# Kernel tuning notes

Measured on AMD Instinct MI355X. Metric: run time of the kernel, lower is better.

Reference implementation:

```python
import jax, jax.numpy as jnp
import numpy as np

B, SEQ, D, H = 16, 100, 128, 8
NS = SEQ + 1
HD = D // H
LN_EPS = 1e-5
NEG_INF = -1e9
GAMMA = 1.0


def setup_inputs() -> dict:
    key = jax.random.key(0)
    ks = jax.random.split(key, 16)
    s = 1.0 / np.sqrt(D)
    return {
        "desc_embeddings": jax.random.normal(ks[0], (B, SEQ, D), jnp.float32),
        "name_value_embeddings": jax.random.normal(ks[1], (B, NS, D), jnp.float32),
        "mask_M": jax.random.uniform(ks[2], (B, H, SEQ, SEQ), jnp.float32),
        "Wq": jax.random.normal(ks[3], (D, D), jnp.float32) * s,
        "bq": jnp.zeros((D,), jnp.float32),
        "Wk": jax.random.normal(ks[4], (D, D), jnp.float32) * s,
        "bk": jnp.zeros((D,), jnp.float32),
        "Wv": jax.random.normal(ks[5], (D, D), jnp.float32) * s,
        "bv": jnp.zeros((D,), jnp.float32),
        "W1": jax.random.normal(ks[6], (D, 2 * D), jnp.float32) * s,  # edge_update lin1
        "b1": jnp.zeros((D,), jnp.float32),
        "ln_g": jnp.ones((D,), jnp.float32),
        "ln_b": jnp.zeros((D,), jnp.float32),
        "W2": jax.random.normal(ks[7], (D, D), jnp.float32) * s,  # edge_update lin2
        "b2": jnp.zeros((D,), jnp.float32),
        "Wa": jax.random.normal(ks[8], (1, 3 * HD), jnp.float32) * s,  # attn_proj
        "ba": jnp.zeros((1,), jnp.float32),
    }


def _layernorm(x, g, b):
    mu = x.mean(-1, keepdims=True)
    var = ((x - mu) ** 2).mean(-1, keepdims=True)
    return (x - mu) * jax.lax.rsqrt(var + LN_EPS) * g + b


def reference(desc_embeddings, name_value_embeddings, mask_M,
              Wq, bq, Wk, bk, Wv, bv, W1, b1, ln_g, ln_b, W2, b2, Wa, ba):
    # structural adjacency: CLS->Var on, Var->CLS off, Var-Var without self loops
    var_adj = 1.0 - jnp.eye(SEQ, dtype=jnp.float32)
    adj = jnp.zeros((NS, NS), jnp.float32)
    adj = adj.at[1:, 1:].set(var_adj).at[0, 1:].set(1.0)  # [NS, NS]

    def proj(W, b_):
        return (name_value_embeddings @ W.T + b_).reshape(B, NS, H, HD).transpose(0, 2, 1, 3)

    q, k, v = proj(Wq, bq), proj(Wk, bk), proj(Wv, bv)  # [B, H, NS, HD]

    # edge features: broadcast-concat of desc embeddings, [B, NS, NS, 2D]
    d = desc_embeddings
    var_edge = jnp.concatenate([
        jnp.broadcast_to(d[:, :, None, :], (B, SEQ, SEQ, D)),
        jnp.broadcast_to(d[:, None, :, :], (B, SEQ, SEQ, D))], axis=-1)
    cls_edge = jnp.concatenate([d, d], axis=-1)  # [B, SEQ, 2D]
    edge = jnp.zeros((B, NS, NS, 2 * D), jnp.float32)
    edge = edge.at[:, 1:, 1:].set(var_edge).at[:, 0, 1:].set(cls_edge).at[:, 1:, 0].set(cls_edge)

    # edge_update MLP: Linear -> LayerNorm -> ReLU -> Linear
    h = _layernorm(edge @ W1.T + b1, ln_g, ln_b)
    e = jax.nn.relu(h) @ W2.T + b2  # [B, NS, NS, D]
    e = e.reshape(B, NS, NS, H, HD).transpose(0, 3, 1, 2, 4)  # [B, H, NS, NS, HD]
    e = e * adj[None, None, :, :, None]

    qke = jnp.concatenate([
        jnp.broadcast_to(q[:, :, :, None, :], (B, H, NS, NS, HD)),
        jnp.broadcast_to(k[:, :, None, :, :], (B, H, NS, NS, HD)),
        e], axis=-1)  # [B, H, NS, NS, 3*HD]
    qke = jax.nn.leaky_relu(qke, 0.01)  # gat_v2
    logits = jnp.einsum('bhijd,d->bhij', qke, Wa[0]) + ba[0]

    # mask_M probability -> logit bias on Var-Var block
    p = jnp.clip(mask_M, 1e-6, 1.0 - 1e-6)
    bias = (jnp.log(p) - jnp.log1p(-p)) * GAMMA
    logits = logits.at[:, :, 1:, 1:].add(bias)

    logits = logits + jnp.where(adj == 0, NEG_INF, 0.0)[None, None]
    attn = jax.nn.softmax(logits, axis=-1)  # [B, H, NS, NS]
    ctx = jnp.einsum('bhij,bhjd->bhid', attn, v)
    basis = ctx.transpose(0, 2, 1, 3)  # [B, NS, H, HD]
    return basis, attn
```

## Files before the change

kernel.cpp:

```cpp
#include <hip/hip_runtime.h>
#include <hip/hip_bf16.h>

namespace {

constexpr int kB = 16;
constexpr int kSEQ = 100;
constexpr int kNS = 101;
constexpr int kD = 128;
constexpr int kH = 8;

typedef __attribute__((ext_vector_type(8))) __bf16 bf16x8;
typedef __attribute__((ext_vector_type(4))) float f32x4;

__device__ __forceinline__ unsigned short f2bf(float f) {
  union { float f; unsigned int u; } c;
  c.f = f;
  unsigned int u = c.u;
  u += 0x7FFFu + ((u >> 16) & 1u);
  return (unsigned short)(u >> 16);
}

__device__ __forceinline__ float leaky(float x) {
  return x > 0.f ? x : 0.01f * x;
}

__device__ __forceinline__ bf16x8 pack8(const float* y) {
  bf16x8 r;
  r[0] = (__bf16)y[0]; r[1] = (__bf16)y[1];
  r[2] = (__bf16)y[2]; r[3] = (__bf16)y[3];
  r[4] = (__bf16)y[4]; r[5] = (__bf16)y[5];
  r[6] = (__bf16)y[6]; r[7] = (__bf16)y[7];
  return r;
}

__global__ __launch_bounds__(256) void k_front(
    const float* __restrict__ nve,
    const float* __restrict__ Wq, const float* __restrict__ bq,
    const float* __restrict__ Wk, const float* __restrict__ bk,
    const float* __restrict__ Wv, const float* __restrict__ bv,
    const float* __restrict__ Wa,
    const float* __restrict__ desc, const float* __restrict__ W1,
    const float* __restrict__ b1, const float* __restrict__ W2,
    float* __restrict__ v, float* __restrict__ sq, float* __restrict__ sk,
    float* __restrict__ U, float* __restrict__ Qm,
    float* __restrict__ su_, float* __restrict__ nu_,
    float* __restrict__ sw_, float* __restrict__ nw_,
    unsigned short* __restrict__ W2bf) {
  __shared__ float X[8][128];
  __shared__ float part[4][4][4];
  const int bid = blockIdx.x;
  const int tid = threadIdx.x;

  if (bid < 208) {
    const int b = bid / 13;
    const int n0 = (bid % 13) * 8;
    const int d = tid & 127, rh = tid >> 7;
    {
      int r = tid >> 5, c = (tid & 31) * 4;
      int n = n0 + r; if (n > 100) n = 100;
      *(float4*)&X[r][c] = *(const float4*)&nve[((size_t)(b * kNS + n)) * kD + c];
    }
    __syncthreads();

    float aq[4], ak[4], av[4];
    const float bqv = bq[d], bkv = bk[d], bvv = bv[d];
    #pragma unroll
    for (int r = 0; r < 4; ++r) { aq[r] = bqv; ak[r] = bkv; av[r] = bvv; }

    const float* wqr = Wq + (size_t)d * kD;
    const float* wkr = Wk + (size_t)d * kD;
    const float* wvr = Wv + (size_t)d * kD;
    for (int kk = 0; kk < kD; ++kk) {
      float wq = wqr[kk], wk = wkr[kk], wv = wvr[kk];
      #pragma unroll
      for (int r = 0; r < 4; ++r) {
        float x = X[rh * 4 + r][kk];
        aq[r] += wq * x;
        ak[r] += wk * x;
        av[r] += wv * x;
      }
    }

    const int t = d & 15, h = d >> 4;
    const float waq = Wa[t], wak = Wa[16 + t];
    #pragma unroll
    for (int r = 0; r < 4; ++r) {
      int n = n0 + rh * 4 + r;
      if (n < kNS) {
        v[((size_t)(b * kNS + n)) * kD + d] = av[r];
        float cq = leaky(aq[r]) * waq;
        float ck = leaky(ak[r]) * wak;
        cq += __shfl_xor(cq, 1); ck += __shfl_xor(ck, 1);
        cq += __shfl_xor(cq, 2); ck += __shfl_xor(ck, 2);
        cq += __shfl_xor(cq, 4); ck += __shfl_xor(ck, 4);
        cq += __shfl_xor(cq, 8); ck += __shfl_xor(ck, 8);
        if (t == 0) {
          sq[(b * kH + h) * kNS + n] = cq;
          sk[(b * kH + h) * kNS + n] = ck;
        }
      }
    }
  } else if (bid < 416) {
    const int id = bid - 208;
    const int b = id / 13;
    const int s0 = (id % 13) * 8;
    const int d = tid & 127, rh = tid >> 7;
    const int lane = tid & 63, wv = tid >> 6;
    {
      int r = tid >> 5, c = (tid & 31) * 4;
      int s = s0 + r; if (s > 99) s = 99;
      *(float4*)&X[r][c] = *(const float4*)&desc[((size_t)(b * kSEQ + s)) * kD + c];
    }
    __syncthreads();

    float aU[4], aQ[4];
    const float b1v = b1[d];
    #pragma unroll
    for (int r = 0; r < 4; ++r) { aU[r] = b1v; aQ[r] = 0.f; }

    const float* w1r = W1 + (size_t)d * (2 * kD);
    for (int kk = 0; kk < kD; ++kk) {
      float wa = w1r[kk], wb = w1r[kD + kk];
      #pragma unroll
      for (int r = 0; r < 4; ++r) {
        float x = X[rh * 4 + r][kk];
        aU[r] += wa * x;
        aQ[r] += wb * x;
      }
    }
    #pragma unroll
    for (int r = 0; r < 4; ++r) {
      int s = s0 + rh * 4 + r;
      if (s < kSEQ) {
        size_t base = ((size_t)(b * kSEQ + s)) * kD + d;
        U[base] = aU[r];
        Qm[base] = aQ[r];
      }
    }
    #pragma unroll
    for (int r = 0; r < 4; ++r) {
      float s1 = aU[r], s2 = aU[r] * aU[r], s3 = aQ[r], s4 = aQ[r] * aQ[r];
      #pragma unroll
      for (int m = 1; m < 64; m <<= 1) {
        s1 += __shfl_xor(s1, m);
        s2 += __shfl_xor(s2, m);
        s3 += __shfl_xor(s3, m);
        s4 += __shfl_xor(s4, m);
      }
      if (lane == 0) {
        part[wv][r][0] = s1; part[wv][r][1] = s2;
        part[wv][r][2] = s3; part[wv][r][3] = s4;
      }
    }
    __syncthreads();
    if (tid < 32) {
      int r = tid & 7, st = tid >> 3;
      int rh2 = r >> 2, rl = r & 3;
      float val = part[rh2 * 2][rl][st] + part[rh2 * 2 + 1][rl][st];
      int s = s0 + r;
      if (s < kSEQ) {
        float* dst = (st == 0) ? su_ : (st == 1) ? nu_ : (st == 2) ? sw_ : nw_;
        dst[b * kSEQ + s] = val;
      }
    }
  } else {
    int idx = (bid - 416) * 256 + tid;
    W2bf[idx] = f2bf(W2[idx]);
  }
}

__global__ __launch_bounds__(256) void k_g(
    const float* __restrict__ U, const float* __restrict__ Qm,
    float* __restrict__ G) {
  const int it = blockIdx.x;
  const int b = blockIdx.y;
  const int tid = threadIdx.x;
  const int lane = tid & 63, w = tid >> 6;
  const int lr = lane & 15, lg = lane >> 4;

  __shared__ __align__(16) unsigned short Ubf[16 * 128];
  __shared__ __align__(16) unsigned short Qbf[112 * 128];

  {
    int f = tid * 8;
    int row = f >> 7, col = f & 127;
    int i1 = it * 16 + row; if (i1 > 99) i1 = 99;
    const float* src = &U[((size_t)(b * kSEQ + i1)) * kD + col];
    float y[8];
    *(float4*)&y[0] = *(const float4*)&src[0];
    *(float4*)&y[4] = *(const float4*)&src[4];
    *(bf16x8*)&Ubf[row * 128 + ((((col >> 3) ^ (row & 15))) << 3)] = pack8(y);
  }
  for (int itr = 0; itr < 7; ++itr) {
    int f = (itr * 256 + tid) * 8;
    int row = f >> 7, col = f & 127;
    int j1 = row; if (j1 > 99) j1 = 99;
    const float* src = &Qm[((size_t)(b * kSEQ + j1)) * kD + col];
    float y[8];
    *(float4*)&y[0] = *(const float4*)&src[0];
    *(float4*)&y[4] = *(const float4*)&src[4];
    *(bf16x8*)&Qbf[row * 128 + ((((col >> 3) ^ (row & 15))) << 3)] = pack8(y);
  }
  __syncthreads();

  bf16x8 Af[4];
  #pragma unroll
  for (int ks = 0; ks < 4; ++ks) {
    int g8 = (ks * 4 + lg) ^ (lr & 15);
    Af[ks] = *(const bf16x8*)&Ubf[lr * 128 + g8 * 8];
  }
  for (int pass = 0; pass < 2; ++pass) {
    int nth = w + pass * 4;
    if (nth >= 7) break;
    int brow = nth * 16 + lr;
    f32x4 acc = {0.f, 0.f, 0.f, 0.f};
    #pragma unroll
    for (int ks = 0; ks < 4; ++ks) {
      int g8 = (ks * 4 + lg) ^ (brow & 15);
      bf16x8 Bf = *(const bf16x8*)&Qbf[brow * 128 + g8 * 8];
      acc = __builtin_amdgcn_mfma_f32_16x16x32_bf16(Af[ks], Bf, acc, 0, 0, 0);
    }
    #pragma unroll
    for (int r = 0; r < 4; ++r) {
      int i1 = it * 16 + 4 * lg + r;
      if (i1 <= 99)
        G[((size_t)(b * kSEQ + i1)) * 112 + nth * 16 + lr] = acc[r];
    }
  }
}

__global__ __launch_bounds__(256) void k_mid(
    const float* __restrict__ U, const float* __restrict__ Qm,
    const float* __restrict__ G,
    const float* __restrict__ su_, const float* __restrict__ nu_,
    const float* __restrict__ sw_, const float* __restrict__ nw_,
    const unsigned short* __restrict__ W2bf,
    const float* __restrict__ lng, const float* __restrict__ lnb,
    const float* __restrict__ b2, const float* __restrict__ Wa,
    float* __restrict__ SE) {
  const int bid = blockIdx.x;
  const int tid = threadIdx.x;
  const int lane = tid & 63, w = tid >> 6;
  const int lr = lane & 15, lg = lane >> 4;

  __shared__ __align__(16) unsigned short W2sh[128 * 128];
  __shared__ __align__(16) float gsh[128], bsh[128], b2sh[128];
  __shared__ float SEsh0[16][8];

  #pragma unroll
  for (int itr = 0; itr < 8; ++itr) {
    uint4 val = ((const uint4*)W2bf)[itr * 256 + tid];
    int f = (itr * 256 + tid) * 8;
    int row = f >> 7, g8 = (f >> 3) & 15;
    *(uint4*)&W2sh[row * 128 + ((g8 ^ (row & 15)) << 3)] = val;
  }
  if (tid < 128) {
    gsh[tid] = lng[tid];
    b2sh[tid] = b2[tid];
  } else {
    bsh[tid - 128] = lnb[tid - 128];
  }

  if (bid < 1600) {
    const int i0 = bid % 100;
    const int b = bid / 100;

    const float* Urow = U + ((size_t)(b * kSEQ + i0)) * kD;
    float Ureg[32];
    #pragma unroll
    for (int ks = 0; ks < 4; ++ks) {
      int off = ks * 32 + lg * 8;
      *(float4*)&Ureg[ks * 8] = *(const float4*)&Urow[off];
      *(float4*)&Ureg[ks * 8 + 4] = *(const float4*)&Urow[off + 4];
    }
    const float suv = su_[b * kSEQ + i0], nuv = nu_[b * kSEQ + i0];
    float wa4[4];
    *(float4*)wa4 = *(const float4*)&Wa[32 + 4 * lg];
    __syncthreads();

    #pragma unroll
    for (int t = 0; t < 2; ++t) {
      const int jt = w + t * 4;
      if (jt > 6) break;
      const int j1 = jt * 16 + lr;
      const int j1c = j1 > 99 ? 99 : j1;
      const float swv = sw_[b * kSEQ + j1c];
      const float nwv = nw_[b * kSEQ + j1c];
      const float gv = G[((size_t)(b * kSEQ + i0)) * 112 + j1c];
      const float mean = (suv + swv) * (1.f / 128.f);
      const float ex2 = (nuv + nwv + 2.f * gv) * (1.f / 128.f);
      const float var = ex2 - mean * mean;
      const float rstd = rsqrtf(var + 1e-5f);
      const float amul = rstd, aadd = -mean * rstd;

      bf16x8 Bf[4];
      const float* Qrow = Qm + ((size_t)(b * kSEQ + j1c)) * kD;
      #pragma unroll
      for (int ks = 0; ks < 4; ++ks) {
        const int off = ks * 32 + lg * 8;
        float qv[8], gg[8], bb[8], ys[8];
        *(float4*)&qv[0] = *(const float4*)&Qrow[off];
        *(float4*)&qv[4] = *(const float4*)&Qrow[off + 4];
        *(float4*)&gg[0] = *(const float4*)&gsh[off];
        *(float4*)&gg[4] = *(const float4*)&gsh[off + 4];
        *(float4*)&bb[0] = *(const float4*)&bsh[off];
        *(float4*)&bb[4] = *(const float4*)&bsh[off + 4];
        #pragma unroll
        for (int ee = 0; ee < 8; ++ee) {
          float x = Ureg[ks * 8 + ee] + qv[ee];
          float tt = __builtin_fmaf(x, amul, aadd);
          ys[ee] = fmaxf(__builtin_fmaf(tt, gg[ee], bb[ee]), 0.f);
        }
        Bf[ks] = pack8(ys);
      }

      #pragma unroll
      for (int h = 0; h < 8; ++h) {
        f32x4 acc = *(const f32x4*)&b2sh[h * 16 + 4 * lg];
        #pragma unroll
        for (int ks = 0; ks < 4; ++ks) {
          const int row = h * 16 + lr;
          const int g8 = (ks * 4 + lg) ^ lr;
          bf16x8 Af = *(const bf16x8*)&W2sh[row * 128 + g8 * 8];
          acc = __builtin_amdgcn_mfma_f32_16x16x32_bf16(Af, Bf[ks], acc, 0, 0, 0);
        }
        float s = 0.f;
        #pragma unroll
        for (int r = 0; r < 4; ++r) s += leaky(acc[r]) * wa4[r];
        s += __shfl_xor(s, 16);
        s += __shfl_xor(s, 32);
        if (lane < 16 && j1 <= 99)
          SE[(((size_t)(b * kH + h)) * kNS + (i0 + 1)) * kNS + (j1 + 1)] = s;
      }
    }
  } else {
    const int id = bid - 1600;
    const int jt = id % 7;
    const int b = id / 7;

    const int j1 = jt * 16 + lr;
    const int j1c = j1 > 99 ? 99 : j1;
    const float* Urow = U + ((size_t)(b * kSEQ + j1c)) * kD;
    const float* Qrow = Qm + ((size_t)(b * kSEQ + j1c)) * kD;
    float Xreg[32];
    #pragma unroll
    for (int ks = 0; ks < 4; ++ks) {
      int off = ks * 32 + lg * 8;
      float4 ua = *(const float4*)&Urow[off];
      float4 ub = *(const float4*)&Urow[off + 4];
      float4 qa = *(const float4*)&Qrow[off];
      float4 qb = *(const float4*)&Qrow[off + 4];
      Xreg[ks * 8 + 0] = ua.x + qa.x; Xreg[ks * 8 + 1] = ua.y + qa.y;
      Xreg[ks * 8 + 2] = ua.z + qa.z; Xreg[ks * 8 + 3] = ua.w + qa.w;
      Xreg[ks * 8 + 4] = ub.x + qb.x; Xreg[ks * 8 + 5] = ub.y + qb.y;
      Xreg[ks * 8 + 6] = ub.z + qb.z; Xreg[ks * 8 + 7] = ub.w + qb.w;
    }
    float amul, aadd;
    {
      float mean = (su_[b * kSEQ + j1c] + sw_[b * kSEQ + j1c]) * (1.f / 128.f);
      float gd = G[((size_t)(b * kSEQ + j1c)) * 112 + j1c];
      float ex2 = (nu_[b * kSEQ + j1c] + nw_[b * kSEQ + j1c] + 2.f * gd) * (1.f / 128.f);
      float var = ex2 - mean * mean;
      float rstd = rsqrtf(var + 1e-5f);
      amul = rstd; aadd = -mean * rstd;
    }
    __syncthreads();

    bf16x8 Af[4];
    #pragma unroll
    for (int ks = 0; ks < 4; ++ks) {
      float ys[8], gg[8], bb[8];
      const int off = ks * 32 + lg * 8;
      *(float4*)&gg[0] = *(const float4*)&gsh[off];
      *(float4*)&gg[4] = *(const float4*)&gsh[off + 4];
      *(float4*)&bb[0] = *(const float4*)&bsh[off];
      *(float4*)&bb[4] = *(const float4*)&bsh[off + 4];
      #pragma unroll
      for (int ee = 0; ee < 8; ++ee) {
        float t = __builtin_fmaf(Xreg[ks * 8 + ee], amul, aadd);
        ys[ee] = fmaxf(__builtin_fmaf(t, gg[ee], bb[ee]), 0.f);
      }
      Af[ks] = pack8(ys);
    }

    const float waE = Wa[32 + lr];
    #pragma unroll
    for (int n = 0; n < 2; ++n) {
      const int nt = 2 * w + n;
      const int brow = nt * 16 + lr;
      f32x4 acc = {0.f, 0.f, 0.f, 0.f};
      #pragma unroll
      for (int ks = 0; ks < 4; ++ks) {
        int g8 = (ks * 4 + lg) ^ (brow & 15);
        bf16x8 Bf = *(const bf16x8*)&W2sh[brow * 128 + g8 * 8];
        acc = __builtin_amdgcn_mfma_f32_16x16x32_bf16(Af[ks], Bf, acc, 0, 0, 0);
      }
      const float b2v = b2sh[nt * 16 + lr];
      #pragma unroll
      for (int r = 0; r < 4; ++r) {
        float y = acc[r] + b2v;
        float c = leaky(y) * waE;
        c += __shfl_xor(c, 1);
        c += __shfl_xor(c, 2);
        c += __shfl_xor(c, 4);
        c += __shfl_xor(c, 8);
        if (lr == 0) SEsh0[4 * lg + r][nt] = c;
      }
    }
    __syncthreads();
    if (tid < 128) {
      int rowloc = tid & 15, h = tid >> 4;
      int j1o = jt * 16 + rowloc;
      if (j1o <= 99)
        SE[(((size_t)(b * kH + h)) * kNS) * kNS + (j1o + 1)] = SEsh0[rowloc][h];
    }
  }
}

__global__ __launch_bounds__(512) void k_sm(
    const float* __restrict__ sq, const float* __restrict__ sk,
    const float* __restrict__ v, const float* __restrict__ maskM,
    const float* __restrict__ ba,
    float* __restrict__ basis, float* __restrict__ attn) {
  const int h = blockIdx.x;
  const int b = blockIdx.y;
  const int half = blockIdx.z;
  const int tid = threadIdx.x;
  const int lane = tid & 63, w = tid >> 6;

  __shared__ float vsh[101][17];
  __shared__ float scr[8][104];

  for (int j = tid >> 4; j < kNS; j += 32)
    vsh[j][tid & 15] = v[((size_t)(b * kNS + j)) * kD + h * 16 + (tid & 15)];
  __syncthreads();

  const float bav = ba[0];
  const int skbase = (b * kH + h) * kNS;
  const int iend = half * 51 + 51 < kNS ? half * 51 + 51 : kNS;
  for (int i = half * 51 + w; i < iend; i += 8) {
    const float sqv = sq[skbase + i];
    float* arow = attn + (((size_t)(b * kH + h)) * kNS + i) * kNS;
    const int j1 = lane + 1;
    const int j2 = lane + 65;
    const bool val1 = (j1 != i);
    const bool val2 = (j2 <= 100) && (j2 != i);
    float l1 = -1e30f, l2 = -1e30f;
    {
      float lgt = sqv + sk[skbase + j1] + arow[j1] + bav;
      if (i >= 1) {
        float p = maskM[(((size_t)(b * kH + h)) * kSEQ + (i - 1)) * kSEQ + (j1 - 1)];
        p = fminf(fmaxf(p, 1e-6f), 1.f - 1e-6f);
        lgt += __logf(__fdividef(p, 1.f - p));
      }
      if (val1) l1 = lgt;
    }
    if (val2) {
      float lgt = sqv + sk[skbase + j2] + arow[j2] + bav;
      if (i >= 1) {
        float p = maskM[(((size_t)(b * kH + h)) * kSEQ + (i - 1)) * kSEQ + (j2 - 1)];
        p = fminf(fmaxf(p, 1e-6f), 1.f - 1e-6f);
        lgt += __logf(__fdividef(p, 1.f - p));
      }
      l2 = lgt;
    }
    float mx = fmaxf(l1, l2);
    #pragma unroll
    for (int m = 1; m < 64; m <<= 1) mx = fmaxf(mx, __shfl_xor(mx, m));
    float e1 = __expf(l1 - mx);
    float e2 = __expf(l2 - mx);
    float sm = e1 + e2;
    #pragma unroll
    for (int m = 1; m < 64; m <<= 1) sm += __shfl_xor(sm, m);
    float inv = 1.f / sm;
    float a1 = e1 * inv, a2 = e2 * inv;
    arow[j1] = a1;
    scr[w][j1] = a1;
    if (lane < 36) {
      arow[j2] = a2;
      scr[w][j2] = a2;
    }
    if (lane == 0) arow[0] = 0.f;

    const int g = lane >> 4, t = lane & 15;
    float accc = 0.f;
    #pragma unroll 5
    for (int jj = 0; jj < 25; ++jj) {
      int j = 1 + g + jj * 4;
      accc += scr[w][j] * vsh[j][t];
    }
    accc += __shfl_xor(accc, 16);
    accc += __shfl_xor(accc, 32);
    if (lane < 16) basis[(((size_t)(b * kNS + i)) * kH + h) * 16 + t] = accc;
  }
}

}

extern "C" void kernel_launch(void* const* d_in, const int* in_sizes, int n_in,
                              void* d_out, int out_size, void* d_ws,
                              size_t ws_size, hipStream_t stream) {
  const float* desc = (const float*)d_in[0];
  const float* nve = (const float*)d_in[1];
  const float* maskM = (const float*)d_in[2];
  const float* Wq = (const float*)d_in[3];
  const float* bq = (const float*)d_in[4];
  const float* Wk = (const float*)d_in[5];
  const float* bk = (const float*)d_in[6];
  const float* Wv = (const float*)d_in[7];
  const float* bv = (const float*)d_in[8];
  const float* W1 = (const float*)d_in[9];
  const float* b1 = (const float*)d_in[10];
  const float* lng = (const float*)d_in[11];
  const float* lnb = (const float*)d_in[12];
  const float* W2 = (const float*)d_in[13];
  const float* b2 = (const float*)d_in[14];
  const float* Wa = (const float*)d_in[15];
  const float* ba = (const float*)d_in[16];

  float* wsf = (float*)d_ws;
  float* U = wsf;
  float* Qm = U + kB * kSEQ * kD;
  float* vw = Qm + kB * kSEQ * kD;
  float* sqw = vw + kB * kNS * kD;
  float* skw = sqw + kB * kH * kNS;
  float* su_ = skw + kB * kH * kNS;
  float* nu_ = su_ + kB * kSEQ;
  float* sw_ = nu_ + kB * kSEQ;
  float* nw_ = sw_ + kB * kSEQ;
  float* G = nw_ + kB * kSEQ;
  unsigned short* W2bf = (unsigned short*)(G + kB * kSEQ * 112);

  float* basis = (float*)d_out;
  float* attn = basis + (size_t)kB * kNS * kH * 16;
  float* SE = attn;

  k_front<<<dim3(480), 256, 0, stream>>>(nve, Wq, bq, Wk, bk, Wv, bv, Wa,
                                         desc, W1, b1, W2,
                                         vw, sqw, skw, U, Qm,
                                         su_, nu_, sw_, nw_, W2bf);
  k_g<<<dim3(7, kB), 256, 0, stream>>>(U, Qm, G);
  k_mid<<<dim3(1712), 256, 0, stream>>>(U, Qm, G, su_, nu_, sw_, nw_, W2bf,
                                        lng, lnb, b2, Wa, SE);
  k_sm<<<dim3(kH, kB, 2), 512, 0, stream>>>(sqw, skw, vw, maskM, ba,
                                            basis, attn);
}
```

Measured before the change: 74.98 us.

## Fuse edge-MLP logits kernel with softmax/context kernel per query row

New measurement: 92.99 us. +24.0%, slower.

```diff
diff --git a/kernel.cpp b/kernel.cpp
--- a/kernel.cpp
+++ b/kernel.cpp
@@ -229,7 +229,7 @@
   }
 }
 
-__global__ __launch_bounds__(256) void k_mid(
+__global__ __launch_bounds__(256) void k_att(
     const float* __restrict__ U, const float* __restrict__ Qm,
     const float* __restrict__ G,
     const float* __restrict__ su_, const float* __restrict__ nu_,
@@ -237,15 +237,21 @@
     const unsigned short* __restrict__ W2bf,
     const float* __restrict__ lng, const float* __restrict__ lnb,
     const float* __restrict__ b2, const float* __restrict__ Wa,
-    float* __restrict__ SE) {
-  const int bid = blockIdx.x;
+    const float* __restrict__ sq, const float* __restrict__ sk,
+    const float* __restrict__ v, const float* __restrict__ maskM,
+    const float* __restrict__ ba,
+    float* __restrict__ basis, float* __restrict__ attn) {
+  const int i = blockIdx.x;
+  const int b = blockIdx.y;
   const int tid = threadIdx.x;
   const int lane = tid & 63, w = tid >> 6;
   const int lr = lane & 15, lg = lane >> 4;
 
-  __shared__ __align__(16) unsigned short W2sh[128 * 128];
+  __shared__ __align__(16) float smemf[101 * 136];
+  __shared__ float sesh[8][112];
   __shared__ __align__(16) float gsh[128], bsh[128], b2sh[128];
-  __shared__ float SEsh0[16][8];
+  unsigned short* W2sh = (unsigned short*)smemf;
+  float* vsh = smemf;
 
   #pragma unroll
   for (int itr = 0; itr < 8; ++itr) {
@@ -261,184 +267,91 @@
     bsh[tid - 128] = lnb[tid - 128];
   }
 
-  if (bid < 1600) {
-    const int i0 = bid % 100;
-    const int b = bid / 100;
-
-    const float* Urow = U + ((size_t)(b * kSEQ + i0)) * kD;
-    float Ureg[32];
-    #pragma unroll
-    for (int ks = 0; ks < 4; ++ks) {
-      int off = ks * 32 + lg * 8;
-      *(float4*)&Ureg[ks * 8] = *(const float4*)&Urow[off];
-      *(float4*)&Ureg[ks * 8 + 4] = *(const float4*)&Urow[off + 4];
-    }
-    const float suv = su_[b * kSEQ + i0], nuv = nu_[b * kSEQ + i0];
-    float wa4[4];
-    *(float4*)wa4 = *(const float4*)&Wa[32 + 4 * lg];
-    __syncthreads();
-
-    #pragma unroll
-    for (int t = 0; t < 2; ++t) {
-      const int jt = w + t * 4;
-      if (jt > 6) break;
-      const int j1 = jt * 16 + lr;
-      const int j1c = j1 > 99 ? 99 : j1;
-      const float swv = sw_[b * kSEQ + j1c];
-      const float nwv = nw_[b * kSEQ + j1c];
-      const float gv = G[((size_t)(b * kSEQ + i0)) * 112 + j1c];
-      const float mean = (suv + swv) * (1.f / 128.f);
-      const float ex2 = (nuv + nwv + 2.f * gv) * (1.f / 128.f);
-      const float var = ex2 - mean * mean;
-      const float rstd = rsqrtf(var + 1e-5f);
-      const float amul = rstd, aadd = -mean * rstd;
-
-      bf16x8 Bf[4];
-      const float* Qrow = Qm + ((size_t)(b * kSEQ + j1c)) * kD;
-      #pragma unroll
-      for (int ks = 0; ks < 4; ++ks) {
-        const int off = ks * 32 + lg * 8;
-        float qv[8], gg[8], bb[8], ys[8];
-        *(float4*)&qv[0] = *(const float4*)&Qrow[off];
-        *(float4*)&qv[4] = *(const float4*)&Qrow[off + 4];
-        *(float4*)&gg[0] = *(const float4*)&gsh[off];
-        *(float4*)&gg[4] = *(const float4*)&gsh[off + 4];
-        *(float4*)&bb[0] = *(const float4*)&bsh[off];
-        *(float4*)&bb[4] = *(const float4*)&bsh[off + 4];
-        #pragma unroll
-        for (int ee = 0; ee < 8; ++ee) {
-          float x = Ureg[ks * 8 + ee] + qv[ee];
-          float tt = __builtin_fmaf(x, amul, aadd);
-          ys[ee] = fmaxf(__builtin_fmaf(tt, gg[ee], bb[ee]), 0.f);
-        }
-        Bf[ks] = pack8(ys);
-      }
-
-      #pragma unroll
-      for (int h = 0; h < 8; ++h) {
-        f32x4 acc = *(const f32x4*)&b2sh[h * 16 + 4 * lg];
-        #pragma unroll
-        for (int ks = 0; ks < 4; ++ks) {
-          const int row = h * 16 + lr;
-          const int g8 = (ks * 4 + lg) ^ lr;
-          bf16x8 Af = *(const bf16x8*)&W2sh[row * 128 + g8 * 8];
-          acc = __builtin_amdgcn_mfma_f32_16x16x32_bf16(Af, Bf[ks], acc, 0, 0, 0);
-        }
-        float s = 0.f;
-        #pragma unroll
-        for (int r = 0; r < 4; ++r) s += leaky(acc[r]) * wa4[r];
-        s += __shfl_xor(s, 16);
-        s += __shfl_xor(s, 32);
-        if (lane < 16 && j1 <= 99)
-          SE[(((size_t)(b * kH + h)) * kNS + (i0 + 1)) * kNS + (j1 + 1)] = s;
-      }
-    }
-  } else {
-    const int id = bid - 1600;
-    const int jt = id % 7;
-    const int b = id / 7;
-
+  const int i0 = i - 1;
+  const int i0c = i >= 1 ? i0 : 0;
+  const float* UrowI = U + ((size_t)(b * kSEQ + i0c)) * kD;
+  float suv = 0.f, nuv = 0.f;
+  if (i >= 1) {
+    suv = su_[b * kSEQ + i0];
+    nuv = nu_[b * kSEQ + i0];
+  }
+  float wa4[4];
+  *(float4*)wa4 = *(const float4*)&Wa[32 + 4 * lg];
+  __syncthreads();
+
+  for (int t = 0; t < 2; ++t) {
+    const int jt = w + t * 4;
+    if (jt > 6) break;
     const int j1 = jt * 16 + lr;
     const int j1c = j1 > 99 ? 99 : j1;
-    const float* Urow = U + ((size_t)(b * kSEQ + j1c)) * kD;
+    const float* Ur = (i == 0) ? (U + ((size_t)(b * kSEQ + j1c)) * kD) : UrowI;
+    const float sui = (i == 0) ? su_[b * kSEQ + j1c] : suv;
+    const float nui = (i == 0) ? nu_[b * kSEQ + j1c] : nuv;
+    const float gv = (i == 0)
+        ? G[((size_t)(b * kSEQ + j1c)) * 112 + j1c]
+        : G[((size_t)(b * kSEQ + i0c)) * 112 + j1c];
+    const float swv = sw_[b * kSEQ + j1c];
+    const float nwv = nw_[b * kSEQ + j1c];
+    const float mean = (sui + swv) * (1.f / 128.f);
+    const float ex2 = (nui + nwv + 2.f * gv) * (1.f / 128.f);
+    const float var = ex2 - mean * mean;
+    const float rstd = rsqrtf(var + 1e-5f);
+    const float amul = rstd, aadd = -mean * rstd;
+
+    bf16x8 Bf[4];
     const float* Qrow = Qm + ((size_t)(b * kSEQ + j1c)) * kD;
-    float Xreg[32];
     #pragma unroll
     for (int ks = 0; ks < 4; ++ks) {
-      int off = ks * 32 + lg * 8;
-      float4 ua = *(const float4*)&Urow[off];
-      float4 ub = *(const float4*)&Urow[off + 4];
-      float4 qa = *(const float4*)&Qrow[off];
-      float4 qb = *(const float4*)&Qrow[off + 4];
-      Xreg[ks * 8 + 0] = ua.x + qa.x; Xreg[ks * 8 + 1] = ua.y + qa.y;
-      Xreg[ks * 8 + 2] = ua.z + qa.z; Xreg[ks * 8 + 3] = ua.w + qa.w;
-      Xreg[ks * 8 + 4] = ub.x + qb.x; Xreg[ks * 8 + 5] = ub.y + qb.y;
-      Xreg[ks * 8 + 6] = ub.z + qb.z; Xreg[ks * 8 + 7] = ub.w + qb.w;
-    }
-    float amul, aadd;
-    {
-      float mean = (su_[b * kSEQ + j1c] + sw_[b * kSEQ + j1c]) * (1.f / 128.f);
-      float gd = G[((size_t)(b * kSEQ + j1c)) * 112 + j1c];
-      float ex2 = (nu_[b * kSEQ + j1c] + nw_[b * kSEQ + j1c] + 2.f * gd) * (1.f / 128.f);
-      float var = ex2 - mean * mean;
-      float rstd = rsqrtf(var + 1e-5f);
-      amul = rstd; aadd = -mean * rstd;
-    }
-    __syncthreads();
-
-    bf16x8 Af[4];
-    #pragma unroll
-    for (int ks = 0; ks < 4; ++ks) {
-      float ys[8], gg[8], bb[8];
       const int off = ks * 32 + lg * 8;
+      float uv[8], qv[8], gg[8], bb[8], ys[8];
+      *(float4*)&uv[0] = *(const float4*)&Ur[off];
+      *(float4*)&uv[4] = *(const float4*)&Ur[off + 4];
+      *(float4*)&qv[0] = *(const float4*)&Qrow[off];
+      *(float4*)&qv[4] = *(const float4*)&Qrow[off + 4];
       *(float4*)&gg[0] = *(const float4*)&gsh[off];
       *(float4*)&gg[4] = *(const float4*)&gsh[off + 4];
       *(float4*)&bb[0] = *(const float4*)&bsh[off];
       *(float4*)&bb[4] = *(const float4*)&bsh[off + 4];
       #pragma unroll
       for (int ee = 0; ee < 8; ++ee) {
-        float t = __builtin_fmaf(Xreg[ks * 8 + ee], amul, aadd);
-        ys[ee] = fmaxf(__builtin_fmaf(t, gg[ee], bb[ee]), 0.f);
-      }
-      Af[ks] = pack8(ys);
-    }
-
-    const float waE = Wa[32 + lr];
-    #pragma unroll
-    for (int n = 0; n < 2; ++n) {
-      const int nt = 2 * w + n;
-      const int brow = nt * 16 + lr;
-      f32x4 acc = {0.f, 0.f, 0.f, 0.f};
+        float x = uv[ee] + qv[ee];
+        float tt = __builtin_fmaf(x, amul, aadd);
+        ys[ee] = fmaxf(__builtin_fmaf(tt, gg[ee], bb[ee]), 0.f);
+      }
+      Bf[ks] = pack8(ys);
+    }
+
+    #pragma unroll
+    for (int h = 0; h < 8; ++h) {
+      f32x4 acc = *(const f32x4*)&b2sh[h * 16 + 4 * lg];
       #pragma unroll
       for (int ks = 0; ks < 4; ++ks) {
-        int g8 = (ks * 4 + lg) ^ (brow & 15);
-        bf16x8 Bf = *(const bf16x8*)&W2sh[brow * 128 + g8 * 8];
-        acc = __builtin_amdgcn_mfma_f32_16x16x32_bf16(Af[ks], Bf, acc, 0, 0, 0);
-      }
-      const float b2v = b2sh[nt * 16 + lr];
-      #pragma unroll
-      for (int r = 0; r < 4; ++r) {
-        float y = acc[r] + b2v;
-        float c = leaky(y) * waE;
-        c += __shfl_xor(c, 1);
-        c += __shfl_xor(c, 2);
-        c += __shfl_xor(c, 4);
-        c += __shfl_xor(c, 8);
-        if (lr == 0) SEsh0[4 * lg + r][nt] = c;
-      }
-    }
-    __syncthreads();
-    if (tid < 128) {
-      int rowloc = tid & 15, h = tid >> 4;
-      int j1o = jt * 16 + rowloc;
-      if (j1o <= 99)
-        SE[(((size_t)(b * kH + h)) * kNS) * kNS + (j1o + 1)] = SEsh0[rowloc][h];
-    }
-  }
-}
-
-__global__ __launch_bounds__(512) void k_sm(
-    const float* __restrict__ sq, const float* __restrict__ sk,
-    const float* __restrict__ v, const float* __restrict__ maskM,
-    const float* __restrict__ ba,
-    float* __restrict__ basis, float* __restrict__ attn) {
-  const int h = blockIdx.x;
-  const int b = blockIdx.y;
-  const int half = blockIdx.z;
-  const int tid = threadIdx.x;
-  const int lane = tid & 63, w = tid >> 6;
-
-  __shared__ float vsh[101][17];
-  __shared__ float scr[8][104];
-
-  for (int j = tid >> 4; j < kNS; j += 32)
-    vsh[j][tid & 15] = v[((size_t)(b * kNS + j)) * kD + h * 16 + (tid & 15)];
+        const int row = h * 16 + lr;
+        const int g8 = (ks * 4 + lg) ^ lr;
+        bf16x8 Af = *(const bf16x8*)&W2sh[row * 128 + g8 * 8];
+        acc = __builtin_amdgcn_mfma_f32_16x16x32_bf16(Af, Bf[ks], acc, 0, 0, 0);
+      }
+      float s = 0.f;
+      #pragma unroll
+      for (int r = 0; r < 4; ++r) s += leaky(acc[r]) * wa4[r];
+      s += __shfl_xor(s, 16);
+      s += __shfl_xor(s, 32);
+      if (lane < 16) sesh[h][j1] = s;
+    }
+  }
   __syncthreads();
 
+  for (int q = tid; q < 101 * 32; q += 256) {
+    int j = q >> 5, c = (q & 31) * 4;
+    *(float4*)&vsh[j * 136 + c] = *(const float4*)&v[((size_t)(b * kNS + j)) * kD + c];
+  }
+  __syncthreads();
+
   const float bav = ba[0];
-  const int skbase = (b * kH + h) * kNS;
-  const int iend = half * 51 + 51 < kNS ? half * 51 + 51 : kNS;
-  for (int i = half * 51 + w; i < iend; i += 8) {
+  #pragma unroll
+  for (int hh = 0; hh < 2; ++hh) {
+    const int h = w + hh * 4;
+    const int skbase = (b * kH + h) * kNS;
     const float sqv = sq[skbase + i];
     float* arow = attn + (((size_t)(b * kH + h)) * kNS + i) * kNS;
     const int j1 = lane + 1;
@@ -447,18 +360,18 @@
     const bool val2 = (j2 <= 100) && (j2 != i);
     float l1 = -1e30f, l2 = -1e30f;
     {
-      float lgt = sqv + sk[skbase + j1] + arow[j1] + bav;
+      float lgt = sqv + sk[skbase + j1] + sesh[h][j1 - 1] + bav;
       if (i >= 1) {
-        float p = maskM[(((size_t)(b * kH + h)) * kSEQ + (i - 1)) * kSEQ + (j1 - 1)];
+        float p = maskM[(((size_t)(b * kH + h)) * kSEQ + i0) * kSEQ + (j1 - 1)];
         p = fminf(fmaxf(p, 1e-6f), 1.f - 1e-6f);
         lgt += __logf(__fdividef(p, 1.f - p));
       }
       if (val1) l1 = lgt;
     }
     if (val2) {
-      float lgt = sqv + sk[skbase + j2] + arow[j2] + bav;
+      float lgt = sqv + sk[skbase + j2] + sesh[h][j2 - 1] + bav;
       if (i >= 1) {
-        float p = maskM[(((size_t)(b * kH + h)) * kSEQ + (i - 1)) * kSEQ + (j2 - 1)];
+        float p = maskM[(((size_t)(b * kH + h)) * kSEQ + i0) * kSEQ + (j2 - 1)];
         p = fminf(fmaxf(p, 1e-6f), 1.f - 1e-6f);
         lgt += __logf(__fdividef(p, 1.f - p));
       }
@@ -475,10 +388,10 @@
     float inv = 1.f / sm;
     float a1 = e1 * inv, a2 = e2 * inv;
     arow[j1] = a1;
-    scr[w][j1] = a1;
+    sesh[h][j1 - 1] = a1;
     if (lane < 36) {
       arow[j2] = a2;
-      scr[w][j2] = a2;
+      sesh[h][j2 - 1] = a2;
     }
     if (lane == 0) arow[0] = 0.f;
 
@@ -487,7 +400,7 @@
     #pragma unroll 5
     for (int jj = 0; jj < 25; ++jj) {
       int j = 1 + g + jj * 4;
-      accc += scr[w][j] * vsh[j][t];
+      accc += sesh[h][j - 1] * vsh[j * 136 + h * 16 + t];
     }
     accc += __shfl_xor(accc, 16);
     accc += __shfl_xor(accc, 32);
@@ -533,15 +446,14 @@
 
   float* basis = (float*)d_out;
   float* attn = basis + (size_t)kB * kNS * kH * 16;
-  float* SE = attn;
 
   k_front<<<dim3(480), 256, 0, stream>>>(nve, Wq, bq, Wk, bk, Wv, bv, Wa,
                                          desc, W1, b1, W2,
                                          vw, sqw, skw, U, Qm,
                                          su_, nu_, sw_, nw_, W2bf);
   k_g<<<dim3(7, kB), 256, 0, stream>>>(U, Qm, G);
-  k_mid<<<dim3(1712), 256, 0, stream>>>(U, Qm, G, su_, nu_, sw_, nw_, W2bf,
-                                        lng, lnb, b2, Wa, SE);
-  k_sm<<<dim3(kH, kB, 2), 512, 0, stream>>>(sqw, skw, vw, maskM, ba,
-                                            basis, attn);
-}
+  k_att<<<dim3(kNS, kB), 256, 0, stream>>>(U, Qm, G, su_, nu_, sw_, nw_, W2bf,
+                                           lng, lnb, b2, Wa,
+                                           sqw, skw, vw, maskM, ba,
+                                           basis, attn);
+}
```
